# Kernel tuning notes

Measured on AMD Instinct MI355X. Metric: run time of the kernel, lower is better.

The kernel has to match this reference:

```python
import jax, jax.numpy as jnp
import numpy as np

MXFP_BLOCK = 32
FP32_MIN_NORMAL = 2.0 ** (-126)
# fp8_e4m3 element format params (bit_width=8)
EXP_BITS = 4
MBITS = 8            # mantissa bits incl. sign, used as 2**(MBITS-2) fixed-point scale
EMAX = 8
MAX_NORM = 448.0     # 2**8 * 1.75
SCALE_EMAX = 127.0   # 2**(MXFP_SCALE_BITS-1) - 1
MIN_PEXP = -6.0      # -2**(EXP_BITS-1) + 2


def _round_away(x):
    return jnp.sign(x) * jnp.floor(jnp.abs(x) + 0.5)


def mxfp_quant_lastdim(x):
    """Block-wise MXFP fp8_e4m3 fake quant along the last dim (block=32, no padding needed)."""
    shape = x.shape
    xb = x.reshape(shape[:-1] + (shape[-1] // MXFP_BLOCK, MXFP_BLOCK))
    shared = jnp.max(jnp.abs(xb), axis=-1, keepdims=True)
    zero_mask = (shared == 0).astype(xb.dtype)
    shared_exp = jnp.floor(jnp.log2(shared + FP32_MIN_NORMAL * zero_mask)) - EMAX
    shared_exp = jnp.where(shared_exp > SCALE_EMAX, jnp.nan, shared_exp)
    shared_exp = jnp.maximum(shared_exp, -SCALE_EMAX)
    scale = jnp.exp2(shared_exp)
    v = xb / scale
    # per-element private exponent, fixed-point mantissa rounding
    pexp = jnp.floor(jnp.log2(jnp.abs(v) + (v == 0).astype(v.dtype)))
    pexp = jnp.maximum(pexp, MIN_PEXP)
    pscale = jnp.exp2(pexp)
    m = 2.0 ** (MBITS - 2)  # 64
    q = _round_away(v / pscale * m) * pscale / m
    q = jnp.clip(q, -MAX_NORM, MAX_NORM)
    return (q * scale).reshape(shape)


def setup_inputs() -> dict:
    key = jax.random.key(0)
    k1, k2, k3 = jax.random.split(key, 3)
    B, S, DIN, DOUT = 8, 8192, 1024, 1024
    x = jax.random.normal(k1, (B, S, DIN), dtype=jnp.float32)
    weight = jax.random.normal(k2, (DOUT, DIN), dtype=jnp.float32) * 0.02
    bias = jax.random.normal(k3, (DOUT,), dtype=jnp.float32) * 0.02
    return {"x": x, "weight": weight, "bias": bias}


def reference(x, weight, bias):
    xq = mxfp_quant_lastdim(x)          # per-token blocks along features
    wq = mxfp_quant_lastdim(weight)     # per-output-channel blocks along in_features
    return jnp.einsum('bsd,od->bso', xq, wq) + bias
```

## Files before the change

kernel.cpp:

```cpp
#include <hip/hip_runtime.h>
#include <cstdint>
#include <cstddef>

#define MM 65536
#define NN 1024
#define KK 1024
#define NT 16

typedef __bf16 bf16x8 __attribute__((ext_vector_type(8)));
typedef float f32x4 __attribute__((ext_vector_type(4)));

typedef const __attribute__((address_space(1))) unsigned int* gas_t;
typedef __attribute__((address_space(3))) unsigned int* las_t;

__device__ __forceinline__ void gll16(const void* g, void* l) {
  __builtin_amdgcn_global_load_lds((gas_t)g, (las_t)l, 16, 0, 0);
}

__device__ __forceinline__ float exp2i(int e) {
  return __int_as_float((e + 127) << 23);
}

__device__ __forceinline__ f32x4 mfma(bf16x8 a, bf16x8 b, f32x4 c) {
  return __builtin_amdgcn_mfma_f32_16x16x32_bf16(a, b, c, 0, 0, 0);
}

__global__ __launch_bounds__(256) void mxfp_quant(const float* __restrict__ in,
                                                  unsigned short* __restrict__ out) {
  size_t i = (size_t)blockIdx.x * 256 + threadIdx.x;
  float4 v = ((const float4*)in)[i];
  float a = fmaxf(fmaxf(fabsf(v.x), fabsf(v.y)), fmaxf(fabsf(v.z), fabsf(v.w)));
  a = fmaxf(a, __shfl_xor(a, 1));
  a = fmaxf(a, __shfl_xor(a, 2));
  a = fmaxf(a, __shfl_xor(a, 4));
  int ebits = (int)((__float_as_uint(a) >> 23) & 0xff);
  int se = (ebits > 0 ? ebits : 1) - 127 - 8;
  se = se < -126 ? -126 : se;
  float sinv = exp2i(-se);
  float sc = exp2i(se);

  float e[4] = {v.x, v.y, v.z, v.w};
  unsigned short o[4];
#pragma unroll
  for (int c = 0; c < 4; ++c) {
    float vv = e[c] * sinv;
    int pe = (int)((__float_as_uint(vv) >> 23) & 0xff) - 127;
    pe = pe < -6 ? -6 : pe;
    float r = floorf(fabsf(vv) * exp2i(6 - pe) + 0.5f);
    float q = copysignf(r * exp2i(pe - 6), vv);
    q = fminf(fmaxf(q, -448.f), 448.f);
    float res = q * sc;
    o[c] = (unsigned short)(__float_as_uint(res) >> 16);
  }
  ushort4 ov = {o[0], o[1], o[2], o[3]};
  ((ushort4*)out)[i] = ov;
}

__global__ __launch_bounds__(512, 2) void gemm_bt(const unsigned short* __restrict__ A,
                                                  const unsigned short* __restrict__ B,
                                                  const float* __restrict__ bias,
                                                  float* __restrict__ C) {
  __shared__ unsigned short As[2][2][128 * 64];
  __shared__ unsigned short Bs[2][2][128 * 64];
  const int t = threadIdx.x;
  const int wg = ((blockIdx.x & 7) << 7) | (blockIdx.x >> 3);
  const int m0 = (wg >> 2) << 8;
  const int n0 = (wg & 3) << 8;

  const int lane = t & 63, w = t >> 6;
  const int wm = (w >> 2) << 7;
  const int wn = (w & 3) << 6;
  const int quad = lane >> 4, r16 = lane & 15;

  const int rt = t >> 2;
  const int lc = (t & 3) ^ ((rt >> 1) & 3);
  const unsigned short* Ag = A + (size_t)(m0 + rt) * KK + lc * 8;
  const unsigned short* Bg = B + (size_t)(n0 + rt) * KK + lc * 8;
  char* AsW = (char*)As + t * 16;
  char* BsW = (char*)Bs + t * 16;
  const int swq = (quad ^ ((r16 >> 1) & 3)) << 4;
  const char* AsR = (const char*)As + (wm + r16) * 64 + swq;
  const char* BsR = (const char*)Bs + (wn + r16) * 64 + swq;

#define STG_A(BUF, KH, H, T_)                                              \
  gll16(Ag + (size_t)(H) * 128 * KK + (size_t)(T_) * 64 + (KH) * 32,       \
        AsW + (BUF) * 32768 + (KH) * 16384 + (H) * 8192)
#define STG_B(BUF, KH, H, T_)                                              \
  gll16(Bg + (size_t)(H) * 128 * KK + (size_t)(T_) * 64 + (KH) * 32,       \
        BsW + (BUF) * 32768 + (KH) * 16384 + (H) * 8192)
#define LDA(BUF, KH, MP) \
  (*(const bf16x8*)(AsR + (BUF) * 32768 + (KH) * 16384 + (MP) * 1024))
#define LDB(BUF, KH, NP) \
  (*(const bf16x8*)(BsR + (BUF) * 32768 + (KH) * 16384 + (NP) * 1024))
#define MFMA16(MB)                                              \
  do {                                                          \
    acc[(MB) + 0][0] = mfma(a0, b0, acc[(MB) + 0][0]);          \
    acc[(MB) + 0][1] = mfma(a0, b1, acc[(MB) + 0][1]);          \
    acc[(MB) + 0][2] = mfma(a0, b2, acc[(MB) + 0][2]);          \
    acc[(MB) + 0][3] = mfma(a0, b3, acc[(MB) + 0][3]);          \
    acc[(MB) + 1][0] = mfma(a1, b0, acc[(MB) + 1][0]);          \
    acc[(MB) + 1][1] = mfma(a1, b1, acc[(MB) + 1][1]);          \
    acc[(MB) + 1][2] = mfma(a1, b2, acc[(MB) + 1][2]);          \
    acc[(MB) + 1][3] = mfma(a1, b3, acc[(MB) + 1][3]);          \
    acc[(MB) + 2][0] = mfma(a2, b0, acc[(MB) + 2][0]);          \
    acc[(MB) + 2][1] = mfma(a2, b1, acc[(MB) + 2][1]);          \
    acc[(MB) + 2][2] = mfma(a2, b2, acc[(MB) + 2][2]);          \
    acc[(MB) + 2][3] = mfma(a2, b3, acc[(MB) + 2][3]);          \
    acc[(MB) + 3][0] = mfma(a3, b0, acc[(MB) + 3][0]);          \
    acc[(MB) + 3][1] = mfma(a3, b1, acc[(MB) + 3][1]);          \
    acc[(MB) + 3][2] = mfma(a3, b2, acc[(MB) + 3][2]);          \
    acc[(MB) + 3][3] = mfma(a3, b3, acc[(MB) + 3][3]);          \
  } while (0)

  f32x4 acc[8][4] = {};

  STG_A(0, 0, 0, 0); STG_A(0, 0, 1, 0);
  STG_B(0, 0, 0, 0); STG_B(0, 0, 1, 0);
  STG_A(0, 1, 0, 0); STG_A(0, 1, 1, 0);
  STG_B(0, 1, 0, 0); STG_B(0, 1, 1, 0);

#pragma unroll 2
  for (int kt = 0; kt < NT; ++kt) {
    const int bi = kt & 1;
    const int nx = bi ^ 1;
    const bool pf = (kt + 1) < NT;
    bf16x8 a0, a1, a2, a3, b0, b1, b2, b3;

    if (pf) {
      STG_A(nx, 0, 0, kt + 1); STG_A(nx, 0, 1, kt + 1);
      asm volatile("s_waitcnt vmcnt(6)" ::: "memory");
    } else {
      asm volatile("s_waitcnt vmcnt(4)" ::: "memory");
    }
    __builtin_amdgcn_s_barrier();
    asm volatile("" ::: "memory");
    a0 = LDA(bi, 0, 0); a1 = LDA(bi, 0, 1); a2 = LDA(bi, 0, 2); a3 = LDA(bi, 0, 3);
    b0 = LDB(bi, 0, 0); b1 = LDB(bi, 0, 1); b2 = LDB(bi, 0, 2); b3 = LDB(bi, 0, 3);
    __builtin_amdgcn_s_setprio(1);
    MFMA16(0);
    __builtin_amdgcn_s_setprio(0);
    __builtin_amdgcn_s_barrier();

    a0 = LDA(bi, 0, 4); a1 = LDA(bi, 0, 5); a2 = LDA(bi, 0, 6); a3 = LDA(bi, 0, 7);
    if (pf) { STG_B(nx, 0, 0, kt + 1); STG_B(nx, 0, 1, kt + 1); }
    __builtin_amdgcn_s_barrier();
    __builtin_amdgcn_s_setprio(1);
    MFMA16(4);
    __builtin_amdgcn_s_setprio(0);
    __builtin_amdgcn_s_barrier();

    if (pf) {
      STG_A(nx, 1, 0, kt + 1); STG_A(nx, 1, 1, kt + 1);
      asm volatile("s_waitcnt vmcnt(6)" ::: "memory");
    } else {
      asm volatile("s_waitcnt vmcnt(0)" ::: "memory");
    }
    __builtin_amdgcn_s_barrier();
    asm volatile("" ::: "memory");
    a0 = LDA(bi, 1, 0); a1 = LDA(bi, 1, 1); a2 = LDA(bi, 1, 2); a3 = LDA(bi, 1, 3);
    b0 = LDB(bi, 1, 0); b1 = LDB(bi, 1, 1); b2 = LDB(bi, 1, 2); b3 = LDB(bi, 1, 3);
    __builtin_amdgcn_s_setprio(1);
    MFMA16(0);
    __builtin_amdgcn_s_setprio(0);
    __builtin_amdgcn_s_barrier();

    a0 = LDA(bi, 1, 4); a1 = LDA(bi, 1, 5); a2 = LDA(bi, 1, 6); a3 = LDA(bi, 1, 7);
    if (pf) { STG_B(nx, 1, 0, kt + 1); STG_B(nx, 1, 1, kt + 1); }
    __builtin_amdgcn_s_barrier();
    __builtin_amdgcn_s_setprio(1);
    MFMA16(4);
    __builtin_amdgcn_s_setprio(0);
    __builtin_amdgcn_s_barrier();
  }

  float bcol[4];
#pragma unroll
  for (int j = 0; j < 4; ++j) bcol[j] = bias[n0 + wn + j * 16 + r16];
#pragma unroll
  for (int mp = 0; mp < 8; ++mp) {
    const int rbase = m0 + wm + mp * 16 + quad * 4;
#pragma unroll
    for (int j = 0; j < 4; ++j) {
      const int col = n0 + wn + j * 16 + r16;
      float* Cp = C + (size_t)rbase * NN + col;
#pragma unroll
      for (int reg = 0; reg < 4; ++reg)
        Cp[(size_t)reg * NN] = acc[mp][j][reg] + bcol[j];
    }
  }
#undef STG_A
#undef STG_B
#undef LDA
#undef LDB
#undef MFMA16
}

extern "C" void kernel_launch(void* const* d_in, const int* in_sizes, int n_in,
                              void* d_out, int out_size, void* d_ws, size_t ws_size,
                              hipStream_t stream) {
  const float* x = (const float*)d_in[0];
  const float* wgt = (const float*)d_in[1];
  const float* bias = (const float*)d_in[2];
  float* out = (float*)d_out;

  unsigned short* xq = (unsigned short*)d_ws;
  unsigned short* wq = xq + (size_t)MM * KK;

  mxfp_quant<<<(MM * (size_t)KK) / 1024, 256, 0, stream>>>(x, xq);
  mxfp_quant<<<(NN * (size_t)KK) / 1024, 256, 0, stream>>>(wgt, wq);
  gemm_bt<<<(MM / 256) * (NN / 256), 512, 0, stream>>>(xq, wq, bias, out);
}
```

Before: 580.0 us.

## Software-pipeline LDS fragment loads one cluster ahead of MFMA clusters

Restructures the GEMM main loop so the LDS reads for the next MFMA cluster are issued before the current cluster runs. Separate register sets (aX/aY, bX/bY) double-buffer the fragments, and global prefetches are reissued further ahead, so the first half of tile kt+2 goes into the buffer being consumed. The aim is to hide LDS read latency behind the matrix cores and remove the exposed load-then-compute stalls at each barrier. In exchange it raises register pressure and makes the vmcnt wait counts and the buffer-reuse ordering more fragile.

```diff
diff --git a/kernel.cpp b/kernel.cpp
--- a/kernel.cpp
+++ b/kernel.cpp
@@ -88,90 +88,96 @@
 #define STG_B(BUF, KH, H, T_)                                              \
   gll16(Bg + (size_t)(H) * 128 * KK + (size_t)(T_) * 64 + (KH) * 32,       \
         BsW + (BUF) * 32768 + (KH) * 16384 + (H) * 8192)
-#define LDA(BUF, KH, MP) \
+#define LDA_(BUF, KH, MP) \
   (*(const bf16x8*)(AsR + (BUF) * 32768 + (KH) * 16384 + (MP) * 1024))
-#define LDB(BUF, KH, NP) \
+#define LDB_(BUF, KH, NP) \
   (*(const bf16x8*)(BsR + (BUF) * 32768 + (KH) * 16384 + (NP) * 1024))
-#define MFMA16(MB)                                              \
-  do {                                                          \
-    acc[(MB) + 0][0] = mfma(a0, b0, acc[(MB) + 0][0]);          \
-    acc[(MB) + 0][1] = mfma(a0, b1, acc[(MB) + 0][1]);          \
-    acc[(MB) + 0][2] = mfma(a0, b2, acc[(MB) + 0][2]);          \
-    acc[(MB) + 0][3] = mfma(a0, b3, acc[(MB) + 0][3]);          \
-    acc[(MB) + 1][0] = mfma(a1, b0, acc[(MB) + 1][0]);          \
-    acc[(MB) + 1][1] = mfma(a1, b1, acc[(MB) + 1][1]);          \
-    acc[(MB) + 1][2] = mfma(a1, b2, acc[(MB) + 1][2]);          \
-    acc[(MB) + 1][3] = mfma(a1, b3, acc[(MB) + 1][3]);          \
-    acc[(MB) + 2][0] = mfma(a2, b0, acc[(MB) + 2][0]);          \
-    acc[(MB) + 2][1] = mfma(a2, b1, acc[(MB) + 2][1]);          \
-    acc[(MB) + 2][2] = mfma(a2, b2, acc[(MB) + 2][2]);          \
-    acc[(MB) + 2][3] = mfma(a2, b3, acc[(MB) + 2][3]);          \
-    acc[(MB) + 3][0] = mfma(a3, b0, acc[(MB) + 3][0]);          \
-    acc[(MB) + 3][1] = mfma(a3, b1, acc[(MB) + 3][1]);          \
-    acc[(MB) + 3][2] = mfma(a3, b2, acc[(MB) + 3][2]);          \
-    acc[(MB) + 3][3] = mfma(a3, b3, acc[(MB) + 3][3]);          \
+#define CLOBBER asm volatile("" ::: "memory")
+#define BARRIER do { __builtin_amdgcn_s_barrier(); CLOBBER; } while (0)
+#define CLUSTER(MB, AR, BR)                                       \
+  do {                                                            \
+    __builtin_amdgcn_s_setprio(1);                                \
+    acc[(MB) + 0][0] = mfma(AR[0], BR[0], acc[(MB) + 0][0]);      \
+    acc[(MB) + 0][1] = mfma(AR[0], BR[1], acc[(MB) + 0][1]);      \
+    acc[(MB) + 0][2] = mfma(AR[0], BR[2], acc[(MB) + 0][2]);      \
+    acc[(MB) + 0][3] = mfma(AR[0], BR[3], acc[(MB) + 0][3]);      \
+    acc[(MB) + 1][0] = mfma(AR[1], BR[0], acc[(MB) + 1][0]);      \
+    acc[(MB) + 1][1] = mfma(AR[1], BR[1], acc[(MB) + 1][1]);      \
+    acc[(MB) + 1][2] = mfma(AR[1], BR[2], acc[(MB) + 1][2]);      \
+    acc[(MB) + 1][3] = mfma(AR[1], BR[3], acc[(MB) + 1][3]);      \
+    acc[(MB) + 2][0] = mfma(AR[2], BR[0], acc[(MB) + 2][0]);      \
+    acc[(MB) + 2][1] = mfma(AR[2], BR[1], acc[(MB) + 2][1]);      \
+    acc[(MB) + 2][2] = mfma(AR[2], BR[2], acc[(MB) + 2][2]);      \
+    acc[(MB) + 2][3] = mfma(AR[2], BR[3], acc[(MB) + 2][3]);      \
+    acc[(MB) + 3][0] = mfma(AR[3], BR[0], acc[(MB) + 3][0]);      \
+    acc[(MB) + 3][1] = mfma(AR[3], BR[1], acc[(MB) + 3][1]);      \
+    acc[(MB) + 3][2] = mfma(AR[3], BR[2], acc[(MB) + 3][2]);      \
+    acc[(MB) + 3][3] = mfma(AR[3], BR[3], acc[(MB) + 3][3]);      \
+    __builtin_amdgcn_s_setprio(0);                                \
   } while (0)
 
+#define TILE(BI, NX, KT, PF1, PF2, VM0, VM2)                              \
+  do {                                                                    \
+                                                        \
+    aY[0] = LDA_(BI, 0, 4); aY[1] = LDA_(BI, 0, 5);                       \
+    aY[2] = LDA_(BI, 0, 6); aY[3] = LDA_(BI, 0, 7);                       \
+    if (PF1) { STG_A(NX, 1, 0, (KT) + 1); STG_A(NX, 1, 1, (KT) + 1); }    \
+    asm volatile("s_waitcnt vmcnt(" VM0 ")" ::: "memory");                \
+    BARRIER;                                                              \
+    CLUSTER(0, aX, bX);                                                   \
+    BARRIER;                                                              \
+                                                        \
+    aX[0] = LDA_(BI, 1, 0); aX[1] = LDA_(BI, 1, 1);                       \
+    aX[2] = LDA_(BI, 1, 2); aX[3] = LDA_(BI, 1, 3);                       \
+    bY[0] = LDB_(BI, 1, 0); bY[1] = LDB_(BI, 1, 1);                       \
+    bY[2] = LDB_(BI, 1, 2); bY[3] = LDB_(BI, 1, 3);                       \
+    if (PF1) { STG_B(NX, 1, 0, (KT) + 1); STG_B(NX, 1, 1, (KT) + 1); }    \
+    BARRIER;                                                              \
+    CLUSTER(4, aY, bX);                                                   \
+    BARRIER;                                                              \
+                                                        \
+    aY[0] = LDA_(BI, 1, 4); aY[1] = LDA_(BI, 1, 5);                       \
+    aY[2] = LDA_(BI, 1, 6); aY[3] = LDA_(BI, 1, 7);                       \
+    if (PF2) { STG_A(BI, 0, 0, (KT) + 2); STG_A(BI, 0, 1, (KT) + 2); }    \
+    asm volatile("s_waitcnt vmcnt(" VM2 ")" ::: "memory");                \
+    BARRIER;                                                              \
+    CLUSTER(0, aX, bY);                                                   \
+    BARRIER;                                                              \
+                                                        \
+    if (PF1) {                                                            \
+      aX[0] = LDA_(NX, 0, 0); aX[1] = LDA_(NX, 0, 1);                     \
+      aX[2] = LDA_(NX, 0, 2); aX[3] = LDA_(NX, 0, 3);                     \
+      bX[0] = LDB_(NX, 0, 0); bX[1] = LDB_(NX, 0, 1);                     \
+      bX[2] = LDB_(NX, 0, 2); bX[3] = LDB_(NX, 0, 3);                     \
+    }                                                                     \
+    if (PF2) { STG_B(BI, 0, 0, (KT) + 2); STG_B(BI, 0, 1, (KT) + 2); }    \
+    BARRIER;                                                              \
+    CLUSTER(4, aY, bY);                                                   \
+    BARRIER;                                                              \
+  } while (0)
+
   f32x4 acc[8][4] = {};
+  bf16x8 aX[4], aY[4], bX[4], bY[4];
 
   STG_A(0, 0, 0, 0); STG_A(0, 0, 1, 0);
   STG_B(0, 0, 0, 0); STG_B(0, 0, 1, 0);
   STG_A(0, 1, 0, 0); STG_A(0, 1, 1, 0);
   STG_B(0, 1, 0, 0); STG_B(0, 1, 1, 0);
-
-#pragma unroll 2
-  for (int kt = 0; kt < NT; ++kt) {
-    const int bi = kt & 1;
-    const int nx = bi ^ 1;
-    const bool pf = (kt + 1) < NT;
-    bf16x8 a0, a1, a2, a3, b0, b1, b2, b3;
-
-    if (pf) {
-      STG_A(nx, 0, 0, kt + 1); STG_A(nx, 0, 1, kt + 1);
-      asm volatile("s_waitcnt vmcnt(6)" ::: "memory");
-    } else {
-      asm volatile("s_waitcnt vmcnt(4)" ::: "memory");
-    }
-    __builtin_amdgcn_s_barrier();
-    asm volatile("" ::: "memory");
-    a0 = LDA(bi, 0, 0); a1 = LDA(bi, 0, 1); a2 = LDA(bi, 0, 2); a3 = LDA(bi, 0, 3);
-    b0 = LDB(bi, 0, 0); b1 = LDB(bi, 0, 1); b2 = LDB(bi, 0, 2); b3 = LDB(bi, 0, 3);
-    __builtin_amdgcn_s_setprio(1);
-    MFMA16(0);
-    __builtin_amdgcn_s_setprio(0);
-    __builtin_amdgcn_s_barrier();
-
-    a0 = LDA(bi, 0, 4); a1 = LDA(bi, 0, 5); a2 = LDA(bi, 0, 6); a3 = LDA(bi, 0, 7);
-    if (pf) { STG_B(nx, 0, 0, kt + 1); STG_B(nx, 0, 1, kt + 1); }
-    __builtin_amdgcn_s_barrier();
-    __builtin_amdgcn_s_setprio(1);
-    MFMA16(4);
-    __builtin_amdgcn_s_setprio(0);
-    __builtin_amdgcn_s_barrier();
-
-    if (pf) {
-      STG_A(nx, 1, 0, kt + 1); STG_A(nx, 1, 1, kt + 1);
-      asm volatile("s_waitcnt vmcnt(6)" ::: "memory");
-    } else {
-      asm volatile("s_waitcnt vmcnt(0)" ::: "memory");
-    }
-    __builtin_amdgcn_s_barrier();
-    asm volatile("" ::: "memory");
-    a0 = LDA(bi, 1, 0); a1 = LDA(bi, 1, 1); a2 = LDA(bi, 1, 2); a3 = LDA(bi, 1, 3);
-    b0 = LDB(bi, 1, 0); b1 = LDB(bi, 1, 1); b2 = LDB(bi, 1, 2); b3 = LDB(bi, 1, 3);
-    __builtin_amdgcn_s_setprio(1);
-    MFMA16(0);
-    __builtin_amdgcn_s_setprio(0);
-    __builtin_amdgcn_s_barrier();
-
-    a0 = LDA(bi, 1, 4); a1 = LDA(bi, 1, 5); a2 = LDA(bi, 1, 6); a3 = LDA(bi, 1, 7);
-    if (pf) { STG_B(nx, 1, 0, kt + 1); STG_B(nx, 1, 1, kt + 1); }
-    __builtin_amdgcn_s_barrier();
-    __builtin_amdgcn_s_setprio(1);
-    MFMA16(4);
-    __builtin_amdgcn_s_setprio(0);
-    __builtin_amdgcn_s_barrier();
+  STG_A(1, 0, 0, 1); STG_A(1, 0, 1, 1);
+  STG_B(1, 0, 0, 1); STG_B(1, 0, 1, 1);
+  asm volatile("s_waitcnt vmcnt(8)" ::: "memory");
+  BARRIER;
+  aX[0] = LDA_(0, 0, 0); aX[1] = LDA_(0, 0, 1);
+  aX[2] = LDA_(0, 0, 2); aX[3] = LDA_(0, 0, 3);
+  bX[0] = LDB_(0, 0, 0); bX[1] = LDB_(0, 0, 1);
+  bX[2] = LDB_(0, 0, 2); bX[3] = LDB_(0, 0, 3);
+
+  for (int kt = 0; kt < NT - 2; kt += 2) {
+    TILE(0, 1, kt, 1, 1, "6", "6");
+    TILE(1, 0, kt + 1, 1, 1, "6", "6");
   }
+  TILE(0, 1, NT - 2, 1, 0, "6", "4");
+  TILE(1, 0, NT - 1, 0, 0, "0", "0");
 
   float bcol[4];
 #pragma unroll
@@ -190,9 +196,12 @@
   }
 #undef STG_A
 #undef STG_B
-#undef LDA
-#undef LDB
-#undef MFMA16
+#undef LDA_
+#undef LDB_
+#undef CLOBBER
+#undef BARRIER
+#undef CLUSTER
+#undef TILE
 }
 
 extern "C" void kernel_launch(void* const* d_in, const int* in_sizes, int n_in,
```

Result: no change. 587.8 us (+1.3%).
